# Kernel tuning notes

Hardware: AMD Instinct MI355X
Metric: run time of the kernel (lower is better)

## Reference

```python
import jax, jax.numpy as jnp
import numpy as np
from itertools import combinations

# Static configuration matching init_kwargs / input_specs
ADD = 3        # max subset size (init arg 'add')
N_COLS = 16    # columns_num = x.shape[1]
BATCH = 262144


def _subset_index_tables(n_cols, add):
    """For each subset size i in [2, min(add, n_cols)], an int array [num_subsets_i, i]
    of column indices, in the same lexicographic order as itertools.combinations
    (identical to the original torch loop order)."""
    tables = []
    for i in range(2, min(add, n_cols) + 1):
        tables.append(np.array(list(combinations(range(n_cols), i)), dtype=np.int32))
    return tables

_IDX_TABLES = _subset_index_tables(N_COLS, ADD)


def setup_inputs() -> dict:
    key = jax.random.key(0)
    x = jax.random.normal(key, (BATCH, N_COLS), dtype=jnp.float32)
    return {"x": x}


def reference(x):
    # Original: for every subset c of columns with 2 <= |c| <= add, append
    # prod(x[:, c], axis=1) to the output, after the original columns.
    outs = [x]
    for idx in _IDX_TABLES:           # idx: [m_i, i]
        # x[:, idx] -> [B, m_i, i]; product over subset members -> [B, m_i]
        outs.append(jnp.prod(x[:, idx], axis=2))
    return jnp.concatenate(outs, axis=1)  # [B, n + sum_i C(n, i)]
```

## Files before the change

### kernel.cpp

```cpp
#include <hip/hip_runtime.h>
#include <cstdint>


#define NCOLS   16
#define NOUT    696
#define RPB     128
#define THREADS 256
#define F4_PER_ROW 174
#define F4_PER_BLOCK (RPB * F4_PER_ROW)
#define ITERS   (F4_PER_BLOCK / THREADS)

typedef float vfloat4 __attribute__((ext_vector_type(4)));

struct Tab { uint32_t v[NOUT]; };
static constexpr Tab make_tab() {
    Tab T{};
    int n = 0;
    for (uint32_t c = 0; c < NCOLS; ++c)
        T.v[n++] = c | (16u << 8) | (16u << 16);
    for (uint32_t i = 0; i < NCOLS; ++i)
        for (uint32_t j = i + 1; j < NCOLS; ++j)
            T.v[n++] = i | (j << 8) | (16u << 16);
    for (uint32_t i = 0; i < NCOLS; ++i)
        for (uint32_t j = i + 1; j < NCOLS; ++j)
            for (uint32_t k = j + 1; k < NCOLS; ++k)
                T.v[n++] = i | (j << 8) | (k << 16);
    return T;
}
__constant__ Tab c_tab = make_tab();

__global__ __launch_bounds__(THREADS) void algebraic_expand_kernel(
        const float* __restrict__ x, float* __restrict__ out, int nrows) {
    __shared__ float    xs[RPB * 17];
    __shared__ uint4    tab4[F4_PER_ROW];

    const int tid = threadIdx.x;
    const int r0  = blockIdx.x * RPB;

    for (int i = tid; i < NOUT; i += THREADS)
        ((uint32_t*)tab4)[i] = c_tab.v[i];

    for (int i = tid; i < RPB * 17; i += THREADS) {
        int r = i / 17;
        int c = i - r * 17;
        float v = 1.0f;
        if (c < NCOLS) {
            int row = r0 + r;
            v = (row < nrows) ? x[row * NCOLS + c] : 0.0f;
        }
        xs[i] = v;
    }
    __syncthreads();

    vfloat4* outv = (vfloat4*)out + (long long)r0 * F4_PER_ROW;
    const long long rows_here = (long long)nrows - r0;
    const long long maxe = (rows_here >= RPB ? (long long)RPB : rows_here) * F4_PER_ROW;

    for (int it = 0; it < ITERS; ++it) {
        const int e = it * THREADS + tid;
        if (e >= maxe) return;
        const int row = (int)((unsigned)e / F4_PER_ROW);
        const int c4  = e - row * F4_PER_ROW;
        const float* __restrict__ xr = xs + row * 17;

        const uint4 t = tab4[c4];
        vfloat4 o;
        o.x = xr[t.x & 0x1f] * xr[(t.x >> 8) & 0x1f] * xr[(t.x >> 16) & 0x1f];
        o.y = xr[t.y & 0x1f] * xr[(t.y >> 8) & 0x1f] * xr[(t.y >> 16) & 0x1f];
        o.z = xr[t.z & 0x1f] * xr[(t.z >> 8) & 0x1f] * xr[(t.z >> 16) & 0x1f];
        o.w = xr[t.w & 0x1f] * xr[(t.w >> 8) & 0x1f] * xr[(t.w >> 16) & 0x1f];

        __builtin_nontemporal_store(o, &outv[e]);
    }
}

extern "C" void kernel_launch(void* const* d_in, const int* in_sizes, int n_in,
                              void* d_out, int out_size, void* d_ws, size_t ws_size,
                              hipStream_t stream) {
    const float* x = (const float*)d_in[0];
    float* out = (float*)d_out;
    const int nrows = in_sizes[0] / NCOLS;
    const int blocks = (nrows + RPB - 1) / RPB;
    algebraic_expand_kernel<<<blocks, THREADS, 0, stream>>>(x, out, nrows);
}
```

Measured before the change: 724.1 us.

## Compute products in registers with compile-time column tables, stage through LDS chunks

Each thread now loads one whole input row into registers with vector loads. Its wavefront computes a fixed compile-time range of output columns, unrolled with constexpr index tables, which removes the runtime table lookups and the indexed shared-memory reads. Results go into a padded LDS buffer in three column chunks and are then drained with coalesced nontemporal stores. The cost is more synchronisation, a larger LDS footprint that may limit occupancy, and code bloat from the template unrolling.

```diff
diff --git a/kernel.cpp b/kernel.cpp
--- a/kernel.cpp
+++ b/kernel.cpp
@@ -1,14 +1,15 @@
 #include <hip/hip_runtime.h>
 #include <cstdint>
+#include <cstddef>
 
 
-#define NCOLS   16
-#define NOUT    696
-#define RPB     128
-#define THREADS 256
-#define F4_PER_ROW 174
-#define F4_PER_BLOCK (RPB * F4_PER_ROW)
-#define ITERS   (F4_PER_BLOCK / THREADS)
+#define NCOLS       16
+#define NOUT        696
+#define F4_PER_ROW  174
+#define RPB         64
+#define THREADS     256
+#define CHUNK       58
+#define ROWPAD      65
 
 typedef float vfloat4 __attribute__((ext_vector_type(4)));
 
@@ -27,51 +28,117 @@
                 T.v[n++] = i | (j << 8) | (k << 16);
     return T;
 }
-__constant__ Tab c_tab = make_tab();
+static constexpr Tab HT = make_tab();
+
+template<int COL>
+__device__ __forceinline__ float prod_col(const float (&x)[NCOLS]) {
+    constexpr uint32_t t = HT.v[COL];
+    constexpr int a = t & 31;
+    constexpr int b = (t >> 8) & 31;
+    constexpr int c = (t >> 16) & 31;
+    float r = x[a];
+    if constexpr (b < NCOLS) r *= x[b];
+    if constexpr (c < NCOLS) r *= x[c];
+    return r;
+}
+
+template<int C, int END, int PBASE>
+struct Emit {
+    static __device__ __forceinline__ void run(const float (&x)[NCOLS],
+                                               vfloat4 (&st)[CHUNK][ROWPAD],
+                                               int lane) {
+        vfloat4 o;
+        o.x = prod_col<4 * C + 0>(x);
+        o.y = prod_col<4 * C + 1>(x);
+        o.z = prod_col<4 * C + 2>(x);
+        o.w = prod_col<4 * C + 3>(x);
+        st[C - PBASE][lane] = o;
+        Emit<C + 1, END, PBASE>::run(x, st, lane);
+    }
+};
+template<int END, int PBASE>
+struct Emit<END, END, PBASE> {
+    static __device__ __forceinline__ void run(const float (&)[NCOLS],
+                                               vfloat4 (&)[CHUNK][ROWPAD], int) {}
+};
+
+template<int PBASE>
+__device__ __forceinline__ void compute_pass(const float (&x)[NCOLS],
+                                             vfloat4 (&st)[CHUNK][ROWPAD],
+                                             int w, int lane) {
+    if      (w == 0) Emit<PBASE +  0, PBASE + 15, PBASE>::run(x, st, lane);
+    else if (w == 1) Emit<PBASE + 15, PBASE + 30, PBASE>::run(x, st, lane);
+    else if (w == 2) Emit<PBASE + 30, PBASE + 44, PBASE>::run(x, st, lane);
+    else             Emit<PBASE + 44, PBASE + 58, PBASE>::run(x, st, lane);
+}
+
+template<int PBASE>
+__device__ __forceinline__ void drain_pass(const vfloat4 (&st)[CHUNK][ROWPAD],
+                                           vfloat4* __restrict__ outv,
+                                           int tid, int rows_left) {
+#pragma unroll
+    for (int d = 0; d < 14; ++d) {
+        const int g  = d * THREADS + tid;
+        const int rl = g / CHUNK;
+        const int c4 = g - rl * CHUNK;
+        if (rl < rows_left)
+            __builtin_nontemporal_store(st[c4][rl],
+                &outv[(size_t)rl * F4_PER_ROW + PBASE + c4]);
+    }
+    {
+        const int g = 14 * THREADS + tid;
+        if (g < CHUNK * RPB) {
+            const int rl = g / CHUNK;
+            const int c4 = g - rl * CHUNK;
+            if (rl < rows_left)
+                __builtin_nontemporal_store(st[c4][rl],
+                    &outv[(size_t)rl * F4_PER_ROW + PBASE + c4]);
+        }
+    }
+}
 
 __global__ __launch_bounds__(THREADS) void algebraic_expand_kernel(
-        const float* __restrict__ x, float* __restrict__ out, int nrows) {
-    __shared__ float    xs[RPB * 17];
-    __shared__ uint4    tab4[F4_PER_ROW];
+        const float* __restrict__ xg, float* __restrict__ out, int nrows) {
+    __shared__ vfloat4 st[CHUNK][ROWPAD];
 
-    const int tid = threadIdx.x;
-    const int r0  = blockIdx.x * RPB;
+    const int tid  = threadIdx.x;
+    const int lane = tid & 63;
+    const int w    = tid >> 6;
+    const int r0   = blockIdx.x * RPB;
 
-    for (int i = tid; i < NOUT; i += THREADS)
-        ((uint32_t*)tab4)[i] = c_tab.v[i];
+    float x[NCOLS];
+    {
+        const int row = r0 + lane;
+        if (row < nrows) {
+            const vfloat4* xr = (const vfloat4*)xg + (size_t)row * 4;
+            const vfloat4 a = xr[0], b = xr[1], c = xr[2], d = xr[3];
+            x[0]  = a.x; x[1]  = a.y; x[2]  = a.z; x[3]  = a.w;
+            x[4]  = b.x; x[5]  = b.y; x[6]  = b.z; x[7]  = b.w;
+            x[8]  = c.x; x[9]  = c.y; x[10] = c.z; x[11] = c.w;
+            x[12] = d.x; x[13] = d.y; x[14] = d.z; x[15] = d.w;
+        } else {
+#pragma unroll
+            for (int i = 0; i < NCOLS; ++i) x[i] = 0.0f;
+        }
+    }
 
-    for (int i = tid; i < RPB * 17; i += THREADS) {
-        int r = i / 17;
-        int c = i - r * 17;
-        float v = 1.0f;
-        if (c < NCOLS) {
-            int row = r0 + r;
-            v = (row < nrows) ? x[row * NCOLS + c] : 0.0f;
-        }
-        xs[i] = v;
-    }
+    vfloat4* outv = (vfloat4*)out + (size_t)r0 * F4_PER_ROW;
+    const int rem = nrows - r0;
+    const int rows_left = rem < RPB ? rem : RPB;
+
+    compute_pass<0>(x, st, w, lane);
+    __syncthreads();
+    drain_pass<0>(st, outv, tid, rows_left);
     __syncthreads();
 
-    vfloat4* outv = (vfloat4*)out + (long long)r0 * F4_PER_ROW;
-    const long long rows_here = (long long)nrows - r0;
-    const long long maxe = (rows_here >= RPB ? (long long)RPB : rows_here) * F4_PER_ROW;
+    compute_pass<CHUNK>(x, st, w, lane);
+    __syncthreads();
+    drain_pass<CHUNK>(st, outv, tid, rows_left);
+    __syncthreads();
 
-    for (int it = 0; it < ITERS; ++it) {
-        const int e = it * THREADS + tid;
-        if (e >= maxe) return;
-        const int row = (int)((unsigned)e / F4_PER_ROW);
-        const int c4  = e - row * F4_PER_ROW;
-        const float* __restrict__ xr = xs + row * 17;
-
-        const uint4 t = tab4[c4];
-        vfloat4 o;
-        o.x = xr[t.x & 0x1f] * xr[(t.x >> 8) & 0x1f] * xr[(t.x >> 16) & 0x1f];
-        o.y = xr[t.y & 0x1f] * xr[(t.y >> 8) & 0x1f] * xr[(t.y >> 16) & 0x1f];
-        o.z = xr[t.z & 0x1f] * xr[(t.z >> 8) & 0x1f] * xr[(t.z >> 16) & 0x1f];
-        o.w = xr[t.w & 0x1f] * xr[(t.w >> 8) & 0x1f] * xr[(t.w >> 16) & 0x1f];
-
-        __builtin_nontemporal_store(o, &outv[e]);
-    }
+    compute_pass<2 * CHUNK>(x, st, w, lane);
+    __syncthreads();
+    drain_pass<2 * CHUNK>(st, outv, tid, rows_left);
 }
 
 extern "C" void kernel_launch(void* const* d_in, const int* in_sizes, int n_in,
```

After: 780.6 us. 1.08x slower.
